# Optimization experiments

Hardware: AMD Instinct MI355X
Metric: run time of the kernel (lower is better)

Reference implementation:

```python
import jax, jax.numpy as jnp
import numpy as np

DIM, QK, PDIM = 256, 16, 64
EPS = 1e-5  # BatchNorm2d / GroupNorm default eps
SCALE = QK ** -0.5


def bn_eval(y, w, b, rm, rv):
    # eval-mode BatchNorm2d folded to per-channel scale+shift
    inv = w / jnp.sqrt(rv + EPS)
    return y * inv[None, :, None, None] + (b - rm * inv)[None, :, None, None]


def setup_inputs() -> dict:
    key = jax.random.key(0)
    ks = jax.random.split(key, 14)
    qkv_out = 2 * QK + PDIM  # 96
    d = {}
    d["x"] = jax.random.normal(ks[0], (4, DIM, 64, 64), jnp.float32)
    # GroupNorm(1, pdim) affine params
    d["gn_w"] = 1.0 + 0.1 * jax.random.normal(ks[1], (PDIM,), jnp.float32)
    d["gn_b"] = 0.1 * jax.random.normal(ks[2], (PDIM,), jnp.float32)
    # qkv Conv2d_BN: 1x1 conv (no bias) + BN
    d["qkv_w"] = 0.05 * jax.random.normal(ks[3], (qkv_out, PDIM), jnp.float32)
    d["qkv_bn_w"] = 1.0 + 0.1 * jax.random.normal(ks[4], (qkv_out,), jnp.float32)
    d["qkv_bn_b"] = 0.1 * jax.random.normal(ks[5], (qkv_out,), jnp.float32)
    d["qkv_rm"] = 0.1 * jax.random.normal(ks[6], (qkv_out,), jnp.float32)
    d["qkv_rv"] = jax.random.uniform(ks[7], (qkv_out,), jnp.float32, 0.5, 1.5)
    # proj Conv2d_BN: 1x1 conv (no bias) + BN (bn_weight_init=0 in torch; use random for nontrivial output)
    d["proj_w"] = 0.05 * jax.random.normal(ks[8], (DIM, DIM), jnp.float32)
    d["proj_bn_w"] = 1.0 + 0.1 * jax.random.normal(ks[9], (DIM,), jnp.float32)
    d["proj_bn_b"] = 0.1 * jax.random.normal(ks[10], (DIM,), jnp.float32)
    d["proj_rm"] = 0.1 * jax.random.normal(ks[11], (DIM,), jnp.float32)
    d["proj_rv"] = jax.random.uniform(ks[12], (DIM,), jnp.float32, 0.5, 1.5)
    return d


def reference(x, gn_w, gn_b, qkv_w, qkv_bn_w, qkv_bn_b, qkv_rm, qkv_rv,
              proj_w, proj_bn_w, proj_bn_b, proj_rm, proj_rv):
    B, C, H, W = x.shape
    N = H * W
    x1, x2 = x[:, :PDIM], x[:, PDIM:]
    # GroupNorm with 1 group: normalize over (C, H, W) per sample
    mu = jnp.mean(x1, axis=(1, 2, 3), keepdims=True)
    var = jnp.var(x1, axis=(1, 2, 3), keepdims=True)
    x1n = (x1 - mu) * jax.lax.rsqrt(var + EPS)
    x1n = x1n * gn_w[None, :, None, None] + gn_b[None, :, None, None]
    # 1x1 conv + BN (eval)
    qkv = bn_eval(jnp.einsum('bchw,oc->bohw', x1n, qkv_w),
                  qkv_bn_w, qkv_bn_b, qkv_rm, qkv_rv)
    q = qkv[:, :QK].reshape(B, QK, N)
    k = qkv[:, QK:2 * QK].reshape(B, QK, N)
    v = qkv[:, 2 * QK:].reshape(B, PDIM, N)
    # attn[b, n, m] = sum_c q[b,c,n] * k[b,c,m]
    attn = jnp.einsum('bcn,bcm->bnm', q, k) * SCALE
    attn = jax.nn.softmax(attn, axis=-1)
    # x1 = v @ attn^T : out[b,p,n] = sum_m v[b,p,m] * attn[b,n,m]
    x1o = jnp.einsum('bpm,bnm->bpn', v, attn).reshape(B, PDIM, H, W)
    y = jnp.concatenate([x1o, x2], axis=1)
    y = jax.nn.silu(y)
    y = bn_eval(jnp.einsum('bchw,oc->bohw', y, proj_w),
                proj_bn_w, proj_bn_b, proj_rm, proj_rv)
    return y
```

## Files before the change

### kernel.cpp

```cpp
#include <hip/hip_runtime.h>
#include <hip/hip_bf16.h>
#include <math.h>

static constexpr int B_ = 4;
static constexpr int C_ = 256;
static constexpr int PD_ = 64;
static constexpr int N_ = 4096;
static constexpr int O96_ = 96;
static constexpr float EPS_ = 1e-5f;
static constexpr float SCALE_ = 0.25f;
static constexpr float LOG2E_ = 1.4426950408889634f;

typedef __attribute__((ext_vector_type(8))) short short8v;
typedef __attribute__((ext_vector_type(4))) float f32x4;

__device__ inline short f2bf(float x) {
    __hip_bfloat16 h = __float2bfloat16(x);
    short r; __builtin_memcpy(&r, &h, 2); return r;
}
__device__ inline float bf2f(short s) {
    union { float f; unsigned u; } v; v.u = ((unsigned)(unsigned short)s) << 16;
    return v.f;
}
__device__ inline unsigned pack_bf2(float lo, float hi) {
    return ((unsigned)(unsigned short)f2bf(hi) << 16) | (unsigned)(unsigned short)f2bf(lo);
}
__device__ inline float silu_(float v) { return v / (1.0f + __expf(-v)); }
__device__ inline float exp2_fast(float x) {
#if __has_builtin(__builtin_amdgcn_exp2f)
    return __builtin_amdgcn_exp2f(x);
#else
    return __expf(x * 0.6931471805599453f);
#endif
}

__global__ __launch_bounds__(256) void k_gnw(const float* __restrict__ x,
        float* __restrict__ part,
        const float* __restrict__ pw,  const float* __restrict__ bnw,
        const float* __restrict__ bnb, const float* __restrict__ rm,
        const float* __restrict__ rv,  short* __restrict__ wbf,
        float* __restrict__ beta) {
    if (blockIdx.x >= 256) {
        const int idx = (blockIdx.x - 256) * 256 + threadIdx.x;
        const int o = idx >> 8, c = idx & 255;
        const float inv = bnw[o] * rsqrtf(rv[o] + EPS_);
        wbf[idx] = f2bf(pw[idx] * inv);
        if (c == 0) beta[o] = bnb[o] - rm[o] * inv;
        return;
    }
    const int blk = blockIdx.x;
    const int b = blk >> 6, c = blk & 63;
    const float* p = x + (size_t)(b * C_ + c) * N_;
    float s = 0.f, q = 0.f;
    for (int i = threadIdx.x; i < N_; i += 256) {
        float v = p[i]; s += v; q += v * v;
    }
    for (int d = 1; d < 64; d <<= 1) {
        s += __shfl_xor(s, d, 64);
        q += __shfl_xor(q, d, 64);
    }
    __shared__ float ls[4], lq[4];
    const int lane = threadIdx.x & 63, wid = threadIdx.x >> 6;
    if (lane == 0) { ls[wid] = s; lq[wid] = q; }
    __syncthreads();
    if (threadIdx.x == 0) {
        part[2 * blk]     = ls[0] + ls[1] + ls[2] + ls[3];
        part[2 * blk + 1] = lq[0] + lq[1] + lq[2] + lq[3];
    }
}

__global__ __launch_bounds__(64) void k_gn_fin(const float* __restrict__ part,
                                               float* __restrict__ stats) {
    const int b = blockIdx.x;
    float s = part[2 * (b * 64 + threadIdx.x)];
    float q = part[2 * (b * 64 + threadIdx.x) + 1];
    for (int d = 1; d < 64; d <<= 1) {
        s += __shfl_xor(s, d, 64);
        q += __shfl_xor(q, d, 64);
    }
    if (threadIdx.x == 0) {
        const float inv_n = 1.0f / (float)(PD_ * N_);
        float mu = s * inv_n;
        float var = q * inv_n - mu * mu;
        stats[2 * b]     = mu;
        stats[2 * b + 1] = rsqrtf(var + EPS_);
    }
}

__global__ __launch_bounds__(512) void k_qkv(const float* __restrict__ x,
        const float* __restrict__ gnw, const float* __restrict__ gnb,
        const float* __restrict__ qw,  const float* __restrict__ bnw,
        const float* __restrict__ bnb, const float* __restrict__ rm,
        const float* __restrict__ rv,  const float* __restrict__ stats,
        short* __restrict__ qT, short* __restrict__ kfrag, short* __restrict__ vfrag) {
    __shared__ float wl[O96_ * PD_];
    __shared__ float binv[O96_], bbeta[O96_];
    const int t = threadIdx.x;
    const int b = blockIdx.x >> 6;
    const int n0 = (blockIdx.x & 63) << 6;
    for (int i = t; i < O96_ * PD_; i += 512) wl[i] = qw[i];
    for (int o = t; o < O96_; o += 512) {
        float inv  = bnw[o] * rsqrtf(rv[o] + EPS_);
        float beta = bnb[o] - rm[o] * inv;
        if (o < 16) { inv *= SCALE_ * LOG2E_; beta *= SCALE_ * LOG2E_; }
        binv[o] = inv; bbeta[o] = beta;
    }
    const float mu = stats[2 * b], rs = stats[2 * b + 1];
    __syncthreads();
    const int nl = t & 63;
    const int n  = n0 + nl;
    const int og = t >> 6;
    float xn[PD_];
    const float* xb = x + (size_t)b * C_ * N_ + n;
    #pragma unroll
    for (int c = 0; c < PD_; ++c)
        xn[c] = (xb[(size_t)c * N_] - mu) * rs * gnw[c] + gnb[c];
    const size_t mblk = (size_t)b * 64 + (n >> 6);
    short* qrow = qT + ((size_t)b * N_ + n) * 16;
    short* kbase = kfrag + mblk * 1024;
    short* vbase = vfrag + mblk * 4096;
    const int mtk  = 2 * ((nl >> 2) & 1) + (nl >> 5);
    const int colk = 4 * ((nl >> 3) & 3) + (nl & 3);
    const int ks = nl >> 5, gv = (nl >> 3) & 3, jv = nl & 7;
    for (int o = og * 12; o < og * 12 + 12; ++o) {
        const float4* wr = (const float4*)&wl[o * PD_];
        float a = 0.f;
        #pragma unroll
        for (int c4 = 0; c4 < 16; ++c4) {
            float4 w4 = wr[c4];
            a += w4.x * xn[4*c4] + w4.y * xn[4*c4+1] + w4.z * xn[4*c4+2] + w4.w * xn[4*c4+3];
        }
        short val = f2bf(a * binv[o] + bbeta[o]);
        if (o < 16) {
            qrow[o] = val;
        } else if (o < 32) {
            const int c = o - 16;
            kbase[((mtk * 2 + (c >> 3)) * 16 + colk) * 8 + (c & 7)] = val;
        } else {
            const int p = o - 32;
            vbase[(((ks * 4 + (p >> 4)) * 64) + gv * 16 + (p & 15)) * 8 + jv] = val;
        }
    }
}

__global__ __launch_bounds__(256) void k_attn(const short* __restrict__ qT,
        const short* __restrict__ kfrag, const short* __restrict__ vfrag,
        short* __restrict__ apart) {
    const int wg  = blockIdx.x;
    const int swz = (wg & 7) * 128 + (wg >> 3);
    const int b   = swz >> 8;
    const int mq  = (swz >> 5) & 7;
    const int nt  = swz & 31;
    const int n0  = nt << 7;

    const int t    = threadIdx.x;
    const int w    = t >> 6;
    const int lane = t & 63;
    const int g    = lane >> 4;
    const int col  = lane & 15;

    const short* qbase = qT + ((size_t)b * N_ + n0 + w * 32 + col) * 16;
    const short* kfb = kfrag + ((size_t)b * 64 + mq * 8) * 1024;
    const short* vfb = vfrag + ((size_t)b * 64 + mq * 8) * 4096;

    short8v a_q0 = 0, a_q1 = 0;
    if (g < 2) {
        a_q0 = *(const short8v*)(qbase + 8 * g);
        a_q1 = *(const short8v*)(qbase + 256 + 8 * g);
    }
    short8v onesf = 0;
    if (col == 0) {
        #pragma unroll
        for (int j = 0; j < 8; ++j) onesf[j] = (short)0x3F80;
    }

    f32x4 acc0[5], acc1[5];
    #pragma unroll
    for (int pt = 0; pt < 5; ++pt) { acc0[pt] = 0.f; acc1[pt] = 0.f; }

    for (int it = 0; it < 8; ++it) {
        const short* kit = kfb + it * 1024;
        const short* vit = vfb + it * 4096;
        short8v kr[4];
        #pragma unroll
        for (int mt = 0; mt < 4; ++mt) {
            kr[mt] = 0;
            if (g < 2) kr[mt] = *(const short8v*)(kit + ((mt * 2 + g) * 16 + col) * 8);
        }
        short8v vpre[8];
        #pragma unroll
        for (int j = 0; j < 8; ++j)
            vpre[j] = *(const short8v*)(vit + (j * 64 + g * 16 + col) * 8);
        f32x4 s[4];
        #pragma unroll
        for (int mt = 0; mt < 4; ++mt) {
            f32x4 z = 0.f;
            s[mt] = __builtin_amdgcn_mfma_f32_16x16x32_bf16(kr[mt], a_q0, z, 0, 0, 0);
        }
        union { unsigned u[4]; short8v v; } p0k0, p0k1, p1k0, p1k1;
        p0k0.u[0] = pack_bf2(exp2_fast(s[0][0]), exp2_fast(s[0][1]));
        p0k0.u[1] = pack_bf2(exp2_fast(s[0][2]), exp2_fast(s[0][3]));
        p0k0.u[2] = pack_bf2(exp2_fast(s[2][0]), exp2_fast(s[2][1]));
        p0k0.u[3] = pack_bf2(exp2_fast(s[2][2]), exp2_fast(s[2][3]));
        p0k1.u[0] = pack_bf2(exp2_fast(s[1][0]), exp2_fast(s[1][1]));
        p0k1.u[1] = pack_bf2(exp2_fast(s[1][2]), exp2_fast(s[1][3]));
        p0k1.u[2] = pack_bf2(exp2_fast(s[3][0]), exp2_fast(s[3][1]));
        p0k1.u[3] = pack_bf2(exp2_fast(s[3][2]), exp2_fast(s[3][3]));
        #pragma unroll
        for (int mt = 0; mt < 4; ++mt) {
            f32x4 z = 0.f;
            s[mt] = __builtin_amdgcn_mfma_f32_16x16x32_bf16(kr[mt], a_q1, z, 0, 0, 0);
        }
        p1k0.u[0] = pack_bf2(exp2_fast(s[0][0]), exp2_fast(s[0][1]));
        p1k0.u[1] = pack_bf2(exp2_fast(s[0][2]), exp2_fast(s[0][3]));
        p1k0.u[2] = pack_bf2(exp2_fast(s[2][0]), exp2_fast(s[2][1]));
        p1k0.u[3] = pack_bf2(exp2_fast(s[2][2]), exp2_fast(s[2][3]));
        p1k1.u[0] = pack_bf2(exp2_fast(s[1][0]), exp2_fast(s[1][1]));
        p1k1.u[1] = pack_bf2(exp2_fast(s[1][2]), exp2_fast(s[1][3]));
        p1k1.u[2] = pack_bf2(exp2_fast(s[3][0]), exp2_fast(s[3][1]));
        p1k1.u[3] = pack_bf2(exp2_fast(s[3][2]), exp2_fast(s[3][3]));
        acc0[4] = __builtin_amdgcn_mfma_f32_16x16x32_bf16(p0k0.v, onesf, acc0[4], 0, 0, 0);
        acc0[4] = __builtin_amdgcn_mfma_f32_16x16x32_bf16(p0k1.v, onesf, acc0[4], 0, 0, 0);
        acc1[4] = __builtin_amdgcn_mfma_f32_16x16x32_bf16(p1k0.v, onesf, acc1[4], 0, 0, 0);
        acc1[4] = __builtin_amdgcn_mfma_f32_16x16x32_bf16(p1k1.v, onesf, acc1[4], 0, 0, 0);
        #pragma unroll
        for (int pt = 0; pt < 4; ++pt) {
            acc0[pt] = __builtin_amdgcn_mfma_f32_16x16x32_bf16(p0k0.v, vpre[pt],     acc0[pt], 0, 0, 0);
            acc0[pt] = __builtin_amdgcn_mfma_f32_16x16x32_bf16(p0k1.v, vpre[4 + pt], acc0[pt], 0, 0, 0);
            acc1[pt] = __builtin_amdgcn_mfma_f32_16x16x32_bf16(p1k0.v, vpre[pt],     acc1[pt], 0, 0, 0);
            acc1[pt] = __builtin_amdgcn_mfma_f32_16x16x32_bf16(p1k1.v, vpre[4 + pt], acc1[pt], 0, 0, 0);
        }
    }
    short* po = apart + (size_t)((b * 8 + mq) * 32 + nt) * 8448;
    #pragma unroll
    for (int pt = 0; pt < 4; ++pt) {
        #pragma unroll
        for (int r = 0; r < 4; ++r) {
            po[(w * 32 + 4 * g + r) * 64 + pt * 16 + col]      = f2bf(acc0[pt][r]);
            po[(w * 32 + 16 + 4 * g + r) * 64 + pt * 16 + col] = f2bf(acc1[pt][r]);
        }
    }
    if (col == 0) {
        float* ms = (float*)(po + 8192);
        #pragma unroll
        for (int r = 0; r < 4; ++r) {
            ms[w * 32 + 4 * g + r]      = acc0[4][r];
            ms[w * 32 + 16 + 4 * g + r] = acc1[4][r];
        }
    }
}

__global__ __launch_bounds__(256) void k_proj2(const short* __restrict__ apart,
        const float* __restrict__ x, const short* __restrict__ wbf,
        const float* __restrict__ beta, float* __restrict__ out) {
    __shared__ __align__(16) short ybf[32 * 256];
    const int t  = threadIdx.x;
    const int nt = blockIdx.x;
    const int b  = blockIdx.y;
    const int n0 = nt << 5;

    {
        const int nn = t >> 3, pg = t & 7;
        const int qloc = ((nt & 3) << 5) + nn;
        const short* pbase = apart + (size_t)((b * 8) * 32 + (nt >> 2)) * 8448;
        float oacc[8] = {0.f, 0.f, 0.f, 0.f, 0.f, 0.f, 0.f, 0.f};
        float Ssum = 0.f;
        #pragma unroll
        for (int k = 0; k < 8; ++k) {
            const short* pk = pbase + (size_t)k * 32 * 8448;
            Ssum += ((const float*)(pk + 8192))[qloc];
            short8v a = *(const short8v*)(pk + qloc * 64 + pg * 8);
            #pragma unroll
            for (int j = 0; j < 8; ++j) oacc[j] += bf2f(a[j]);
        }
        const float inv = 1.0f / Ssum;
        const int slot = pg ^ (nn & 7);
        *(uint4*)(ybf + nn * 256 + slot * 8) = make_uint4(
            pack_bf2(silu_(oacc[0] * inv), silu_(oacc[1] * inv)),
            pack_bf2(silu_(oacc[2] * inv), silu_(oacc[3] * inv)),
            pack_bf2(silu_(oacc[4] * inv), silu_(oacc[5] * inv)),
            pack_bf2(silu_(oacc[6] * inv), silu_(oacc[7] * inv)));
    }
    {
        const int nn = t & 31, cg = t >> 5;
        #pragma unroll
        for (int s3 = 0; s3 < 3; ++s3) {
            const int cb = 64 + cg * 24 + s3 * 8;
            unsigned pk4[4];
            #pragma unroll
            for (int j = 0; j < 4; ++j) {
                float v0 = x[((size_t)(b * C_ + cb + 2 * j)) * N_ + n0 + nn];
                float v1 = x[((size_t)(b * C_ + cb + 2 * j + 1)) * N_ + n0 + nn];
                pk4[j] = pack_bf2(silu_(v0), silu_(v1));
            }
            const int slot = (8 + cg * 3 + s3) ^ (nn & 7);
            *(uint4*)(ybf + nn * 256 + slot * 8) = make_uint4(pk4[0], pk4[1], pk4[2], pk4[3]);
        }
    }
    __syncthreads();
    const int w = t >> 6, lane = t & 63;
    const int col = lane & 15, g = lane >> 4;
    const int o_base = w << 6;
    f32x4 acc[4][2];
    #pragma unroll
    for (int ot = 0; ot < 4; ++ot) { acc[ot][0] = 0.f; acc[ot][1] = 0.f; }
    #pragma unroll
    for (int kk = 0; kk < 8; ++kk) {
        short8v bf0 = *(const short8v*)(ybf + col * 256 + (((kk * 4 + g) ^ (col & 7)) << 3));
        short8v bf1 = *(const short8v*)(ybf + (16 + col) * 256 + (((kk * 4 + g) ^ (col & 7)) << 3));
        #pragma unroll
        for (int ot = 0; ot < 4; ++ot) {
            short8v af = *(const short8v*)(wbf + (size_t)(o_base + ot * 16 + col) * C_ + kk * 32 + g * 8);
            acc[ot][0] = __builtin_amdgcn_mfma_f32_16x16x32_bf16(af, bf0, acc[ot][0], 0, 0, 0);
            acc[ot][1] = __builtin_amdgcn_mfma_f32_16x16x32_bf16(af, bf1, acc[ot][1], 0, 0, 0);
        }
    }
    #pragma unroll
    for (int ot = 0; ot < 4; ++ot) {
        #pragma unroll
        for (int r = 0; r < 4; ++r) {
            const int o = o_base + ot * 16 + 4 * g + r;
            const float be = beta[o];
            float* po = out + ((size_t)(b * C_ + o)) * N_ + n0 + col;
            po[0]  = acc[ot][0][r] + be;
            po[16] = acc[ot][1][r] + be;
        }
    }
}

extern "C" void kernel_launch(void* const* d_in, const int* in_sizes, int n_in,
                              void* d_out, int out_size, void* d_ws, size_t ws_size,
                              hipStream_t stream) {
    const float* x   = (const float*)d_in[0];
    const float* gnw = (const float*)d_in[1];
    const float* gnb = (const float*)d_in[2];
    const float* qw  = (const float*)d_in[3];
    const float* qbw = (const float*)d_in[4];
    const float* qbb = (const float*)d_in[5];
    const float* qrm = (const float*)d_in[6];
    const float* qrv = (const float*)d_in[7];
    const float* pw  = (const float*)d_in[8];
    const float* pbw = (const float*)d_in[9];
    const float* pbb = (const float*)d_in[10];
    const float* prm = (const float*)d_in[11];
    const float* prv = (const float*)d_in[12];
    float* out = (float*)d_out;
    char* wsb = (char*)d_ws;

    float* part  = (float*)wsb;
    float* stats = (float*)(wsb + 2048);
    short* wbf   = (short*)(wsb + 4096);
    float* beta  = (float*)(wsb + 135168);
    short* qTb   = (short*)(wsb + 139264);
    short* kfrag = (short*)(wsb + 663552);
    short* vfrag = (short*)(wsb + 1187840);
    short* apart = (short*)(wsb + 3284992);

    k_gnw<<<512, 256, 0, stream>>>(x, part, pw, pbw, pbb, prm, prv, wbf, beta);
    k_gn_fin<<<4, 64, 0, stream>>>(part, stats);
    k_qkv<<<256, 512, 0, stream>>>(x, gnw, gnb, qw, qbw, qbb, qrm, qrv, stats, qTb, kfrag, vfrag);
    k_attn<<<1024, 256, 0, stream>>>(qTb, kfrag, vfrag, apart);
    k_proj2<<<dim3(128, 4), 256, 0, stream>>>(apart, x, wbf, beta, out);
}
```

Baseline: 68.03 us.

## Fold GN finalize into qkv, double-buffer K loads, halve proj tile

Removes the separate GroupNorm finalize launch: each qkv block now reduces the per-sample partial sums itself into shared memory. The attention loop double-buffers K fragment loads so the next iteration's K is fetched while the current one computes. The projection kernel's tile drops from 32 to 16 positions, doubling the grid to raise occupancy and parallelism at the cost of reloading weights more often. The redundant stat reduction in every qkv block adds a little work, and each proj block now does less MFMA work per weight fetch.

```diff
diff --git a/kernel.cpp b/kernel.cpp
--- a/kernel.cpp
+++ b/kernel.cpp
@@ -69,35 +69,33 @@
     }
 }
 
-__global__ __launch_bounds__(64) void k_gn_fin(const float* __restrict__ part,
-                                               float* __restrict__ stats) {
-    const int b = blockIdx.x;
-    float s = part[2 * (b * 64 + threadIdx.x)];
-    float q = part[2 * (b * 64 + threadIdx.x) + 1];
-    for (int d = 1; d < 64; d <<= 1) {
-        s += __shfl_xor(s, d, 64);
-        q += __shfl_xor(q, d, 64);
-    }
-    if (threadIdx.x == 0) {
-        const float inv_n = 1.0f / (float)(PD_ * N_);
-        float mu = s * inv_n;
-        float var = q * inv_n - mu * mu;
-        stats[2 * b]     = mu;
-        stats[2 * b + 1] = rsqrtf(var + EPS_);
-    }
-}
-
 __global__ __launch_bounds__(512) void k_qkv(const float* __restrict__ x,
         const float* __restrict__ gnw, const float* __restrict__ gnb,
         const float* __restrict__ qw,  const float* __restrict__ bnw,
         const float* __restrict__ bnb, const float* __restrict__ rm,
-        const float* __restrict__ rv,  const float* __restrict__ stats,
+        const float* __restrict__ rv,  const float* __restrict__ part,
         short* __restrict__ qT, short* __restrict__ kfrag, short* __restrict__ vfrag) {
     __shared__ float wl[O96_ * PD_];
     __shared__ float binv[O96_], bbeta[O96_];
+    __shared__ float musr[2];
     const int t = threadIdx.x;
     const int b = blockIdx.x >> 6;
     const int n0 = (blockIdx.x & 63) << 6;
+    if (t < 64) {
+        float s = part[2 * (b * 64 + t)];
+        float q = part[2 * (b * 64 + t) + 1];
+        for (int d = 1; d < 64; d <<= 1) {
+            s += __shfl_xor(s, d, 64);
+            q += __shfl_xor(q, d, 64);
+        }
+        if (t == 0) {
+            const float inv_n = 1.0f / (float)(PD_ * N_);
+            float mu = s * inv_n;
+            float var = q * inv_n - mu * mu;
+            musr[0] = mu;
+            musr[1] = rsqrtf(var + EPS_);
+        }
+    }
     for (int i = t; i < O96_ * PD_; i += 512) wl[i] = qw[i];
     for (int o = t; o < O96_; o += 512) {
         float inv  = bnw[o] * rsqrtf(rv[o] + EPS_);
@@ -105,8 +103,8 @@
         if (o < 16) { inv *= SCALE_ * LOG2E_; beta *= SCALE_ * LOG2E_; }
         binv[o] = inv; bbeta[o] = beta;
     }
-    const float mu = stats[2 * b], rs = stats[2 * b + 1];
     __syncthreads();
+    const float mu = musr[0], rs = musr[1];
     const int nl = t & 63;
     const int n  = n0 + nl;
     const int og = t >> 6;
@@ -178,15 +176,17 @@
     #pragma unroll
     for (int pt = 0; pt < 5; ++pt) { acc0[pt] = 0.f; acc1[pt] = 0.f; }
 
-    for (int it = 0; it < 8; ++it) {
+    short8v krA[4], krB[4];
+    auto loadK = [&](short8v (&kr)[4], int it) {
         const short* kit = kfb + it * 1024;
-        const short* vit = vfb + it * 4096;
-        short8v kr[4];
         #pragma unroll
         for (int mt = 0; mt < 4; ++mt) {
             kr[mt] = 0;
             if (g < 2) kr[mt] = *(const short8v*)(kit + ((mt * 2 + g) * 16 + col) * 8);
         }
+    };
+    auto compute = [&](const short8v (&kr)[4], int it) {
+        const short* vit = vfb + it * 4096;
         short8v vpre[8];
         #pragma unroll
         for (int j = 0; j < 8; ++j)
@@ -230,6 +230,14 @@
             acc1[pt] = __builtin_amdgcn_mfma_f32_16x16x32_bf16(p1k0.v, vpre[pt],     acc1[pt], 0, 0, 0);
             acc1[pt] = __builtin_amdgcn_mfma_f32_16x16x32_bf16(p1k1.v, vpre[4 + pt], acc1[pt], 0, 0, 0);
         }
+    };
+
+    loadK(krA, 0);
+    for (int it = 0; it < 8; it += 2) {
+        loadK(krB, it + 1);
+        compute(krA, it);
+        if (it + 2 < 8) loadK(krA, it + 2);
+        compute(krB, it + 1);
     }
     short* po = apart + (size_t)((b * 8 + mq) * 32 + nt) * 8448;
     #pragma unroll
@@ -253,66 +261,59 @@
 __global__ __launch_bounds__(256) void k_proj2(const short* __restrict__ apart,
         const float* __restrict__ x, const short* __restrict__ wbf,
         const float* __restrict__ beta, float* __restrict__ out) {
-    __shared__ __align__(16) short ybf[32 * 256];
+    __shared__ __align__(16) short ybf[16 * 256];
     const int t  = threadIdx.x;
     const int nt = blockIdx.x;
     const int b  = blockIdx.y;
-    const int n0 = nt << 5;
+    const int n0 = nt << 4;
 
     {
-        const int nn = t >> 3, pg = t & 7;
-        const int qloc = ((nt & 3) << 5) + nn;
-        const short* pbase = apart + (size_t)((b * 8) * 32 + (nt >> 2)) * 8448;
-        float oacc[8] = {0.f, 0.f, 0.f, 0.f, 0.f, 0.f, 0.f, 0.f};
+        const int nn = t >> 4, pc = t & 15;
+        const int qloc = ((nt & 7) << 4) + nn;
+        const short* pbase = apart + (size_t)((b * 8) * 32 + (nt >> 3)) * 8448;
+        float o0 = 0.f, o1 = 0.f, o2 = 0.f, o3 = 0.f;
         float Ssum = 0.f;
         #pragma unroll
         for (int k = 0; k < 8; ++k) {
             const short* pk = pbase + (size_t)k * 32 * 8448;
             Ssum += ((const float*)(pk + 8192))[qloc];
-            short8v a = *(const short8v*)(pk + qloc * 64 + pg * 8);
-            #pragma unroll
-            for (int j = 0; j < 8; ++j) oacc[j] += bf2f(a[j]);
+            short4 a = *(const short4*)(pk + qloc * 64 + pc * 4);
+            o0 += bf2f(a.x); o1 += bf2f(a.y); o2 += bf2f(a.z); o3 += bf2f(a.w);
         }
         const float inv = 1.0f / Ssum;
-        const int slot = pg ^ (nn & 7);
-        *(uint4*)(ybf + nn * 256 + slot * 8) = make_uint4(
-            pack_bf2(silu_(oacc[0] * inv), silu_(oacc[1] * inv)),
-            pack_bf2(silu_(oacc[2] * inv), silu_(oacc[3] * inv)),
-            pack_bf2(silu_(oacc[4] * inv), silu_(oacc[5] * inv)),
-            pack_bf2(silu_(oacc[6] * inv), silu_(oacc[7] * inv)));
+        *(uint2*)(ybf + nn * 256 + (((pc >> 1) ^ (nn & 7)) << 3) + ((pc & 1) << 2)) =
+            make_uint2(pack_bf2(silu_(o0 * inv), silu_(o1 * inv)),
+                       pack_bf2(silu_(o2 * inv), silu_(o3 * inv)));
     }
     {
-        const int nn = t & 31, cg = t >> 5;
+        const int nn = t & 15, cg = t >> 4;
         #pragma unroll
         for (int s3 = 0; s3 < 3; ++s3) {
-            const int cb = 64 + cg * 24 + s3 * 8;
-            unsigned pk4[4];
-            #pragma unroll
-            for (int j = 0; j < 4; ++j) {
-                float v0 = x[((size_t)(b * C_ + cb + 2 * j)) * N_ + n0 + nn];
-                float v1 = x[((size_t)(b * C_ + cb + 2 * j + 1)) * N_ + n0 + nn];
-                pk4[j] = pack_bf2(silu_(v0), silu_(v1));
-            }
-            const int slot = (8 + cg * 3 + s3) ^ (nn & 7);
-            *(uint4*)(ybf + nn * 256 + slot * 8) = make_uint4(pk4[0], pk4[1], pk4[2], pk4[3]);
+            const int cb = 64 + cg * 12 + s3 * 4;
+            float v0 = x[((size_t)(b * C_ + cb))     * N_ + n0 + nn];
+            float v1 = x[((size_t)(b * C_ + cb + 1)) * N_ + n0 + nn];
+            float v2 = x[((size_t)(b * C_ + cb + 2)) * N_ + n0 + nn];
+            float v3 = x[((size_t)(b * C_ + cb + 3)) * N_ + n0 + nn];
+            const int ch = 16 + cg * 3 + s3;
+            *(uint2*)(ybf + nn * 256 + (((ch >> 1) ^ (nn & 7)) << 3) + ((ch & 1) << 2)) =
+                make_uint2(pack_bf2(silu_(v0), silu_(v1)),
+                           pack_bf2(silu_(v2), silu_(v3)));
         }
     }
     __syncthreads();
     const int w = t >> 6, lane = t & 63;
     const int col = lane & 15, g = lane >> 4;
     const int o_base = w << 6;
-    f32x4 acc[4][2];
-    #pragma unroll
-    for (int ot = 0; ot < 4; ++ot) { acc[ot][0] = 0.f; acc[ot][1] = 0.f; }
+    f32x4 acc[4];
+    #pragma unroll
+    for (int ot = 0; ot < 4; ++ot) acc[ot] = 0.f;
     #pragma unroll
     for (int kk = 0; kk < 8; ++kk) {
-        short8v bf0 = *(const short8v*)(ybf + col * 256 + (((kk * 4 + g) ^ (col & 7)) << 3));
-        short8v bf1 = *(const short8v*)(ybf + (16 + col) * 256 + (((kk * 4 + g) ^ (col & 7)) << 3));
+        short8v bf = *(const short8v*)(ybf + col * 256 + (((kk * 4 + g) ^ (col & 7)) << 3));
         #pragma unroll
         for (int ot = 0; ot < 4; ++ot) {
             short8v af = *(const short8v*)(wbf + (size_t)(o_base + ot * 16 + col) * C_ + kk * 32 + g * 8);
-            acc[ot][0] = __builtin_amdgcn_mfma_f32_16x16x32_bf16(af, bf0, acc[ot][0], 0, 0, 0);
-            acc[ot][1] = __builtin_amdgcn_mfma_f32_16x16x32_bf16(af, bf1, acc[ot][1], 0, 0, 0);
+            acc[ot] = __builtin_amdgcn_mfma_f32_16x16x32_bf16(af, bf, acc[ot], 0, 0, 0);
         }
     }
     #pragma unroll
@@ -320,10 +321,7 @@
         #pragma unroll
         for (int r = 0; r < 4; ++r) {
             const int o = o_base + ot * 16 + 4 * g + r;
-            const float be = beta[o];
-            float* po = out + ((size_t)(b * C_ + o)) * N_ + n0 + col;
-            po[0]  = acc[ot][0][r] + be;
-            po[16] = acc[ot][1][r] + be;
+            out[((size_t)(b * C_ + o)) * N_ + n0 + col] = acc[ot][r] + beta[o];
         }
     }
 }
@@ -348,7 +346,6 @@
     char* wsb = (char*)d_ws;
 
     float* part  = (float*)wsb;
-    float* stats = (float*)(wsb + 2048);
     short* wbf   = (short*)(wsb + 4096);
     float* beta  = (float*)(wsb + 135168);
     short* qTb   = (short*)(wsb + 139264);
@@ -357,8 +354,7 @@
     short* apart = (short*)(wsb + 3284992);
 
     k_gnw<<<512, 256, 0, stream>>>(x, part, pw, pbw, pbb, prm, prv, wbf, beta);
-    k_gn_fin<<<4, 64, 0, stream>>>(part, stats);
-    k_qkv<<<256, 512, 0, stream>>>(x, gnw, gnb, qw, qbw, qbb, qrm, qrv, stats, qTb, kfrag, vfrag);
+    k_qkv<<<256, 512, 0, stream>>>(x, gnw, gnb, qw, qbw, qbb, qrm, qrv, part, qTb, kfrag, vfrag);
     k_attn<<<1024, 256, 0, stream>>>(qTb, kfrag, vfrag, apart);
-    k_proj2<<<dim3(128, 4), 256, 0, stream>>>(apart, x, wbf, beta, out);
-}
+    k_proj2<<<dim3(256, 4), 256, 0, stream>>>(apart, x, wbf, beta, out);
+}
```

Result: slower. 74.60 us (+9.7%).
